# Optimization experiments

Hardware: AMD Instinct MI355X
Metric: run time of the kernel (lower is better)

Reference implementation:

```python
import jax, jax.numpy as jnp
import numpy as np

N_SCALES = 3
BASE_SIGMA = 0.1
SCALES = jnp.asarray([BASE_SIGMA * 2.0 ** i for i in range(N_SCALES)], dtype=jnp.float32)


def setup_inputs() -> dict:
    key = jax.random.key(0)
    k_x, k_pos, k_tp, k_w1, k_b1, k_w2, k_b2 = jax.random.split(key, 7)
    B, C, T = 16, 306, 4000
    M = 128
    x = jax.random.normal(k_x, (B, C, T), dtype=jnp.float32)
    positions = jax.random.normal(k_pos, (B, C, 2), dtype=jnp.float32)
    target_positions = jax.random.normal(k_tp, (M, 2), dtype=jnp.float32)
    # nn.Linear(3, 32) / nn.Linear(32, 1) params (kaiming-uniform-ish init)
    lim1 = 1.0 / np.sqrt(3.0)
    w1 = jax.random.uniform(k_w1, (3, 32), jnp.float32, -lim1, lim1)
    b1 = jax.random.uniform(k_b1, (32,), jnp.float32, -lim1, lim1)
    lim2 = 1.0 / np.sqrt(32.0)
    w2 = jax.random.uniform(k_w2, (32, 1), jnp.float32, -lim2, lim2)
    b2 = jax.random.uniform(k_b2, (1,), jnp.float32, -lim2, lim2)
    return {"x": x, "positions": positions, "target_positions": target_positions,
            "w1": w1, "b1": b1, "w2": w2, "b2": b2}


def reference(x, positions, target_positions, w1, b1, w2, b2):
    # squared euclidean distances [B, C, M]
    diff = positions[:, :, None, :] - target_positions[None, None, :, :]
    d2 = jnp.sum(diff * diff, axis=-1)
    # multi-scale Gaussian kernels, stacked on last axis -> [B, C, M, n_scales]
    inv = 1.0 / (2.0 * SCALES ** 2)  # [n_scales]
    scale_weights = jnp.exp(-d2[..., None] * inv)
    # tiny 2-layer MLP gate: (3 -> 32 -> 1)
    h = jax.nn.relu(scale_weights @ w1 + b1)  # [B, C, M, 32]
    w = (h @ w2 + b2)[..., 0]                 # [B, C, M]
    # normalize over channel dim
    w = w / (jnp.sum(w, axis=1, keepdims=True) + 1e-8)
    # weighted channel aggregation -> [B, M, T]
    return jnp.einsum('bct,bcm->bmt', x, w)
```

## Files before the change

kernel.cpp:

```cpp
#include <hip/hip_runtime.h>

#define B_ 16
#define C_ 306
#define T_ 4000
#define M_ 128

typedef short bf16x8 __attribute__((ext_vector_type(8)));
typedef float f32x4 __attribute__((ext_vector_type(4)));

#define WF_PER_B 81920

__global__ __launch_bounds__(320)
void gate_kernel(const float* __restrict__ positions,
                 const float* __restrict__ target,
                 const float* __restrict__ w1,
                 const float* __restrict__ b1,
                 const float* __restrict__ w2,
                 const float* __restrict__ b2,
                 unsigned short* __restrict__ wf,
                 float* __restrict__ scale) {
    const int b  = blockIdx.x >> 5;
    const int mg = blockIdx.x & 31;
    const int tid = threadIdx.x;

    __shared__ float s_w1[96], s_b1[32], s_w2[32];
    __shared__ float s_b2;
    __shared__ float s_tgt[8];
    __shared__ float s_part[4][5];
    __shared__ unsigned short s_frag[40 * 72];

    if (tid < 96) s_w1[tid] = w1[tid];
    if (tid < 32) { s_b1[tid] = b1[tid]; s_w2[tid] = w2[tid]; }
    if (tid == 256) s_b2 = b2[0];
    if (tid >= 312) s_tgt[tid - 312] = target[mg * 8 + (tid - 312)];
    __syncthreads();

    float px = 0.0f, py = 0.0f;
    if (tid < C_) {
        px = positions[(b * C_ + tid) * 2 + 0];
        py = positions[(b * C_ + tid) * 2 + 1];
    }

    float wv_[4];
#pragma unroll
    for (int mi = 0; mi < 4; ++mi) {
        float w = 0.0f;
        if (tid < C_) {
            const float dx = px - s_tgt[mi * 2 + 0];
            const float dy = py - s_tgt[mi * 2 + 1];
            const float d2 = dx * dx + dy * dy;
            const float s2 = __expf(-d2 * 3.125f);
            const float q  = s2 * s2;
            const float s1 = q * q;
            const float r  = s1 * s1;
            const float s0 = r * r;
            float acc = s_b2;
#pragma unroll
            for (int j = 0; j < 32; ++j) {
                float h = fmaf(s0, s_w1[j],
                          fmaf(s1, s_w1[32 + j],
                          fmaf(s2, s_w1[64 + j], s_b1[j])));
                acc = fmaf(fmaxf(h, 0.0f), s_w2[j], acc);
            }
            w = acc;
        }
        wv_[mi] = w;
    }

#pragma unroll
    for (int mi = 0; mi < 4; ++mi) {
        float s = wv_[mi];
#pragma unroll
        for (int off = 32; off > 0; off >>= 1) s += __shfl_down(s, off, 64);
        if ((tid & 63) == 0) s_part[mi][tid >> 6] = s;
    }

    const int chunk = tid >> 3;
    const int slot  = tid & 7;
#pragma unroll
    for (int mi = 0; mi < 4; ++mi) {
        const float w = wv_[mi];
        const unsigned int u = __float_as_uint(w);
        const unsigned short h = (unsigned short)(u >> 16);
        const float lof = w - __uint_as_float(u & 0xffff0000u);
        const unsigned short l = (unsigned short)(__float_as_uint(lof) >> 16);
        s_frag[chunk * 72 + mi * 16 + 0 + slot] = h;
        s_frag[chunk * 72 + mi * 16 + 8 + slot] = l;
    }
    __syncthreads();

    if (tid < 4) {
        float tot = s_part[tid][0] + s_part[tid][1] + s_part[tid][2]
                  + s_part[tid][3] + s_part[tid][4];
        scale[b * M_ + mg * 4 + tid] = 1.0f / (tot + 1e-8f);
    }

    {
        const int ch = tid >> 3;
        const int g  = tid & 7;
        const uint4 v = *(const uint4*)(s_frag + ch * 72 + g * 8);
        unsigned short* dst = wf + (size_t)b * WF_PER_B
                            + (size_t)ch * 2048 + mg * 64 + g * 8;
        *(uint4*)dst = v;
    }
}

#define RUNSTRIDE 648

__global__ __launch_bounds__(256, 2)
void merge_gemm(const float* __restrict__ x,
                const unsigned short* __restrict__ wf,
                const float* __restrict__ scale,
                float* __restrict__ out) {
    const int t0 = blockIdx.x * 128;
    const int b  = blockIdx.y;
    const int tid  = threadIdx.x;
    const int lane = tid & 63;
    const int wv   = tid >> 6;
    const int tquad = lane >> 4;
    const int tsub  = lane & 15;

    __shared__ __align__(16) unsigned int sXh[2][4 * RUNSTRIDE];
    __shared__ __align__(16) unsigned int sXl[2][4 * RUNSTRIDE];
    __shared__ __align__(16) float sScale[M_];

    if (tid < M_) sScale[tid] = scale[b * M_ + tid];

    const float* xb = x + (size_t)b * C_ * T_;
    const unsigned short* wfB = wf + (size_t)b * WF_PER_B;

    f32x4 acc[4][4];
#pragma unroll
    for (int i = 0; i < 4; ++i)
#pragma unroll
        for (int j = 0; j < 4; ++j) acc[i][j] = (f32x4){0.f, 0.f, 0.f, 0.f};

    const int mw = (wv & 1) * 64;
    const int tw = (wv >> 1) * 64;

    const int cpB = tid >> 5;
    const int TQ  = tid & 31;
    const float* xcol = xb + min(t0 + TQ * 4, T_ - 4);

    auto loadX = [&](int k, float4* xv) {
#pragma unroll
        for (int sub = 0; sub < 2; ++sub) {
            const int cp = cpB + 8 * sub;
            const int c  = k * 32 + 2 * cp;
            xv[sub * 2 + 0] = *(const float4*)(xcol + (size_t)min(c,     C_ - 1) * T_);
            xv[sub * 2 + 1] = *(const float4*)(xcol + (size_t)min(c + 1, C_ - 1) * T_);
        }
    };
    auto loadW = [&](int k, bf16x8* ah, bf16x8* al) {
#pragma unroll
        for (int mi = 0; mi < 4; ++mi) {
            const size_t aoff = ((size_t)(k * 4 + tquad) * 128
                               + (mw + mi * 16 + tsub)) * 16;
            ah[mi] = *(const bf16x8*)(wfB + aoff);
            al[mi] = *(const bf16x8*)(wfB + aoff + 8);
        }
    };
    auto packX = [&](const float4* xv, unsigned int* Dh, unsigned int* Dl) {
#pragma unroll
        for (int sub = 0; sub < 2; ++sub) {
            const int cp  = cpB + 8 * sub;
            const int run = cp >> 2;
            const int pw  = cp & 3;
            const float* fa = (const float*)&xv[sub * 2 + 0];
            const float* fb = (const float*)&xv[sub * 2 + 1];
            const int base = run * RUNSTRIDE + TQ * 20 + pw;
#pragma unroll
            for (int tt = 0; tt < 4; ++tt) {
                const unsigned int ua = __float_as_uint(fa[tt]);
                const unsigned int ub = __float_as_uint(fb[tt]);
                const float la = fa[tt] - __uint_as_float(ua & 0xffff0000u);
                const float lb = fb[tt] - __uint_as_float(ub & 0xffff0000u);
                Dh[base + tt * 4] = (ua >> 16) | (ub & 0xffff0000u);
                Dl[base + tt * 4] = (__float_as_uint(la) >> 16) |
                                    (__float_as_uint(lb) & 0xffff0000u);
            }
        }
    };

    bf16x8 ah[4], al[4];
    {
        float4 xv[4];
        loadX(0, xv);
        loadW(0, ah, al);
        packX(xv, &sXh[0][0], &sXl[0][0]);
    }
    __syncthreads();

#pragma unroll
    for (int k = 0; k < 10; ++k) {
        float4 xn[4];
        bf16x8 ahn[4], aln[4];
        if (k < 9) {
            loadX(k + 1, xn);
            loadW(k + 1, ahn, aln);
        }

        const unsigned int* Sh = &sXh[k & 1][0];
        const unsigned int* Sl = &sXl[k & 1][0];
        bf16x8 bh[4], bl[4];
#pragma unroll
        for (int i = 0; i < 4; ++i) {
            const int t = tw + i * 16 + tsub;
            const int a = tquad * RUNSTRIDE + (t >> 2) * 20 + (t & 3) * 4;
            bh[i] = *(const bf16x8*)(Sh + a);
            bl[i] = *(const bf16x8*)(Sl + a);
        }

#pragma unroll
        for (int mi = 0; mi < 4; ++mi)
#pragma unroll
            for (int ti = 0; ti < 4; ++ti) {
                acc[mi][ti] = __builtin_amdgcn_mfma_f32_16x16x32_bf16(
                    ah[mi], bh[ti], acc[mi][ti], 0, 0, 0);
                acc[mi][ti] = __builtin_amdgcn_mfma_f32_16x16x32_bf16(
                    ah[mi], bl[ti], acc[mi][ti], 0, 0, 0);
                acc[mi][ti] = __builtin_amdgcn_mfma_f32_16x16x32_bf16(
                    al[mi], bh[ti], acc[mi][ti], 0, 0, 0);
            }

        if (k < 9) {
            packX(xn, &sXh[(k + 1) & 1][0], &sXl[(k + 1) & 1][0]);
            __syncthreads();
#pragma unroll
            for (int mi = 0; mi < 4; ++mi) { ah[mi] = ahn[mi]; al[mi] = aln[mi]; }
        }
    }

#pragma unroll
    for (int mi = 0; mi < 4; ++mi) {
        const int mbase = mw + mi * 16 + tquad * 4;
        const float4 sc = *(const float4*)(sScale + mbase);
        float* op = out + ((size_t)b * M_ + mbase) * T_;
#pragma unroll
        for (int ti = 0; ti < 4; ++ti) {
            const int tg = t0 + tw + ti * 16 + tsub;
            if (tg < T_) {
                op[(size_t)0 * T_ + tg] = acc[mi][ti][0] * sc.x;
                op[(size_t)1 * T_ + tg] = acc[mi][ti][1] * sc.y;
                op[(size_t)2 * T_ + tg] = acc[mi][ti][2] * sc.z;
                op[(size_t)3 * T_ + tg] = acc[mi][ti][3] * sc.w;
            }
        }
    }
}

extern "C" void kernel_launch(void* const* d_in, const int* in_sizes, int n_in,
                              void* d_out, int out_size, void* d_ws, size_t ws_size,
                              hipStream_t stream) {
    const float* x         = (const float*)d_in[0];
    const float* positions = (const float*)d_in[1];
    const float* target    = (const float*)d_in[2];
    const float* w1        = (const float*)d_in[3];
    const float* b1        = (const float*)d_in[4];
    const float* w2        = (const float*)d_in[5];
    const float* b2        = (const float*)d_in[6];
    float* out = (float*)d_out;

    float* scale = (float*)d_ws;
    unsigned short* wf = (unsigned short*)(scale + B_ * M_);

    gate_kernel<<<B_ * 32, 320, 0, stream>>>(positions, target, w1, b1, w2, b2,
                                             wf, scale);

    dim3 grid((T_ + 127) / 128, B_);
    merge_gemm<<<grid, 256, 0, stream>>>(x, wf, scale, out);
}
```

Before: 144.0 us.

## Deepen x prefetch to two stages and reorder MFMA chains in merge GEMM

The merge GEMM now prefetches x two K-steps ahead using two rotating register buffers. The W fragment load moves to after the MFMAs, which removes the duplicate next-step W registers. The three bf16-split MFMA passes are split into separate loops so consecutive MFMAs hit independent accumulators instead of chaining on the same one, and the bf16 packing uses v_perm. __syncthreads is replaced by an explicit lgkmcnt wait plus s_barrier, so the barrier does not also wait on outstanding global loads; the extra prefetch buffer raises register pressure.

```diff
diff --git a/kernel.cpp b/kernel.cpp
--- a/kernel.cpp
+++ b/kernel.cpp
@@ -151,13 +151,13 @@
             xv[sub * 2 + 1] = *(const float4*)(xcol + (size_t)min(c + 1, C_ - 1) * T_);
         }
     };
-    auto loadW = [&](int k, bf16x8* ah, bf16x8* al) {
+    auto loadW = [&](int k, bf16x8* ah_, bf16x8* al_) {
 #pragma unroll
         for (int mi = 0; mi < 4; ++mi) {
             const size_t aoff = ((size_t)(k * 4 + tquad) * 128
                                + (mw + mi * 16 + tsub)) * 16;
-            ah[mi] = *(const bf16x8*)(wfB + aoff);
-            al[mi] = *(const bf16x8*)(wfB + aoff + 8);
+            ah_[mi] = *(const bf16x8*)(wfB + aoff);
+            al_[mi] = *(const bf16x8*)(wfB + aoff + 8);
         }
     };
     auto packX = [&](const float4* xv, unsigned int* Dh, unsigned int* Dl) {
@@ -175,30 +175,26 @@
                 const unsigned int ub = __float_as_uint(fb[tt]);
                 const float la = fa[tt] - __uint_as_float(ua & 0xffff0000u);
                 const float lb = fb[tt] - __uint_as_float(ub & 0xffff0000u);
-                Dh[base + tt * 4] = (ua >> 16) | (ub & 0xffff0000u);
-                Dl[base + tt * 4] = (__float_as_uint(la) >> 16) |
-                                    (__float_as_uint(lb) & 0xffff0000u);
+                Dh[base + tt * 4] = __builtin_amdgcn_perm(ub, ua, 0x07060302u);
+                Dl[base + tt * 4] = __builtin_amdgcn_perm(__float_as_uint(lb),
+                                                          __float_as_uint(la),
+                                                          0x07060302u);
             }
         }
     };
 
     bf16x8 ah[4], al[4];
-    {
-        float4 xv[4];
-        loadX(0, xv);
-        loadW(0, ah, al);
-        packX(xv, &sXh[0][0], &sXl[0][0]);
-    }
-    __syncthreads();
-
-#pragma unroll
-    for (int k = 0; k < 10; ++k) {
-        float4 xn[4];
-        bf16x8 ahn[4], aln[4];
-        if (k < 9) {
-            loadX(k + 1, xn);
-            loadW(k + 1, ahn, aln);
-        }
+    float4 xv0[4], xv1[4];
+    loadX(0, xv0);
+    loadX(1, xv1);
+    loadW(0, ah, al);
+    packX(xv0, &sXh[0][0], &sXl[0][0]);
+    asm volatile("s_waitcnt lgkmcnt(0)" ::: "memory");
+    __builtin_amdgcn_s_barrier();
+    asm volatile("" ::: "memory");
+
+    auto step = [&](const int k, float4 (&xnext)[4], float4 (&xfetch)[4]) {
+        if (k < 8) loadX(k + 2, xfetch);
 
         const unsigned int* Sh = &sXh[k & 1][0];
         const unsigned int* Sl = &sXl[k & 1][0];
@@ -214,21 +210,35 @@
 #pragma unroll
         for (int mi = 0; mi < 4; ++mi)
 #pragma unroll
-            for (int ti = 0; ti < 4; ++ti) {
+            for (int ti = 0; ti < 4; ++ti)
                 acc[mi][ti] = __builtin_amdgcn_mfma_f32_16x16x32_bf16(
                     ah[mi], bh[ti], acc[mi][ti], 0, 0, 0);
+#pragma unroll
+        for (int mi = 0; mi < 4; ++mi)
+#pragma unroll
+            for (int ti = 0; ti < 4; ++ti)
                 acc[mi][ti] = __builtin_amdgcn_mfma_f32_16x16x32_bf16(
                     ah[mi], bl[ti], acc[mi][ti], 0, 0, 0);
+#pragma unroll
+        for (int mi = 0; mi < 4; ++mi)
+#pragma unroll
+            for (int ti = 0; ti < 4; ++ti)
                 acc[mi][ti] = __builtin_amdgcn_mfma_f32_16x16x32_bf16(
                     al[mi], bh[ti], acc[mi][ti], 0, 0, 0);
-            }
 
         if (k < 9) {
-            packX(xn, &sXh[(k + 1) & 1][0], &sXl[(k + 1) & 1][0]);
-            __syncthreads();
-#pragma unroll
-            for (int mi = 0; mi < 4; ++mi) { ah[mi] = ahn[mi]; al[mi] = aln[mi]; }
-        }
+            loadW(k + 1, ah, al);
+            packX(xnext, &sXh[(k + 1) & 1][0], &sXl[(k + 1) & 1][0]);
+            asm volatile("s_waitcnt lgkmcnt(0)" ::: "memory");
+            __builtin_amdgcn_s_barrier();
+            asm volatile("" ::: "memory");
+        }
+    };
+
+#pragma unroll
+    for (int kk = 0; kk < 5; ++kk) {
+        step(2 * kk,     xv1, xv0);
+        step(2 * kk + 1, xv0, xv1);
     }
 
 #pragma unroll
@@ -257,8 +267,9 @@
     const float* target    = (const float*)d_in[2];
     const float* w1        = (const float*)d_in[3];
     const float* b1        = (const float*)d_in[4];
+    const float* b2_dummy  = (const float*)d_in[6];
     const float* w2        = (const float*)d_in[5];
-    const float* b2        = (const float*)d_in[6];
+    const float* b2        = b2_dummy;
     float* out = (float*)d_out;
 
     float* scale = (float*)d_ws;
```

After: 144.9 us. Within noise of the previous version (+0.6%).
